# Kernel tuning notes

Measured on AMD Instinct MI355X. Metric: run time of the kernel, lower is better.

## Reference

```python
import jax, jax.numpy as jnp
import numpy as np

N = 100000      # nodes (cells)
E = 1600000     # edges (kNN graph, avg degree 16)
DIM_IN = 128    # input features per cell
H = 8           # heads
C1 = 8          # per-head channels, layer 1 (concat -> 64)
DIM_OUT = 10    # classes (concat=False -> mean over heads)
NEG_SLOPE = 0.2


def setup_inputs() -> dict:
    key = jax.random.key(0)
    ks = jax.random.split(key, 10)
    s = 0.1
    return {
        "x": jax.random.normal(ks[0], (N, DIM_IN), dtype=jnp.float32),
        "edge_index": jax.random.randint(ks[1], (2, E), 0, N, dtype=jnp.int64),
        "W1": jax.random.normal(ks[2], (DIM_IN, H * C1), dtype=jnp.float32) * s,
        "a_src1": jax.random.normal(ks[3], (H, C1), dtype=jnp.float32) * s,
        "a_dst1": jax.random.normal(ks[4], (H, C1), dtype=jnp.float32) * s,
        "b1": jnp.zeros((H * C1,), dtype=jnp.float32),
        "W2": jax.random.normal(ks[5], (H * C1, H * DIM_OUT), dtype=jnp.float32) * s,
        "a_src2": jax.random.normal(ks[6], (H, DIM_OUT), dtype=jnp.float32) * s,
        "a_dst2": jax.random.normal(ks[7], (H, DIM_OUT), dtype=jnp.float32) * s,
        "b2": jnp.zeros((DIM_OUT,), dtype=jnp.float32),
    }


def _gat_layer(x, src, dst, W, a_src, a_dst, bias, concat, n):
    """PyG-style GATConv: gather -> edge attention -> segment softmax -> scatter."""
    h_, c_ = a_src.shape
    h = (x @ W).reshape(n, h_, c_)                       # [N, H, C]
    alpha_s = jnp.einsum('nhc,hc->nh', h, a_src)         # [N, H]
    alpha_d = jnp.einsum('nhc,hc->nh', h, a_dst)         # [N, H]
    # per-edge logits; PyG: message from src j to dst i, softmax over dst
    e = jax.nn.leaky_relu(alpha_s[src] + alpha_d[dst], NEG_SLOPE)  # [E, H]
    e_max = jax.ops.segment_max(e, dst, num_segments=n)            # [N, H]
    e = jnp.exp(e - e_max[dst])
    denom = jax.ops.segment_sum(e, dst, num_segments=n)            # [N, H]
    alpha = e / denom[dst]                                          # [E, H]
    msg = h[src] * alpha[:, :, None]                                # [E, H, C]
    out = jax.ops.segment_sum(msg, dst, num_segments=n)             # [N, H, C]
    out = out.reshape(n, h_ * c_) if concat else out.mean(axis=1)
    return out + bias


def reference(x, edge_index, W1, a_src1, a_dst1, b1, W2, a_src2, a_dst2, b2):
    n = x.shape[0]
    loops = jnp.arange(n, dtype=edge_index.dtype)
    src = jnp.concatenate([edge_index[0], loops])  # PyG adds self-loops by default
    dst = jnp.concatenate([edge_index[1], loops])
    h = _gat_layer(x, src, dst, W1, a_src1, a_dst1, b1, True, n)   # [N, 64]
    h = jax.nn.elu(h)
    h = _gat_layer(h, src, dst, W2, a_src2, a_dst2, b2, False, n)  # [N, dim_out]
    return jax.nn.log_softmax(h, axis=1)
```

## Files before the change

### kernel.cpp

```cpp
#include <hip/hip_runtime.h>
#include <hip/hip_bf16.h>
#include <cstdint>

#define CAP 64
#define SLICES 8
#define CHUNK_EDGES 8192

__device__ __forceinline__ float lrelu(float v) { return fmaxf(v, 0.2f * v); }

typedef float f32x2 __attribute__((ext_vector_type(2)));
__device__ __forceinline__ float2 q2f(unsigned short u) {
    f32x2 v = __builtin_amdgcn_cvt_pk_f32_fp8((int)u, false);
    return make_float2(v.x, v.y);
}
__device__ __forceinline__ int f2q4(float a, float b, float c, float d) {
    int p = __builtin_amdgcn_cvt_pk_fp8_f32(a, b, 0, false);
    p = __builtin_amdgcn_cvt_pk_fp8_f32(c, d, p, true);
    return p;
}
__device__ __forceinline__ float b2f(unsigned short u) { return __uint_as_float(((unsigned)u) << 16); }
__device__ __forceinline__ unsigned short f2b(float f) {
    unsigned u = __float_as_uint(f);
    return (unsigned short)((u + 0x7FFFu + ((u >> 16) & 1u)) >> 16);
}

__global__ __launch_bounds__(256, 8) void k_bg(const int* __restrict__ ei, int E, int N,
                                               int* __restrict__ cnt, int* __restrict__ bucket,
                                               const float* __restrict__ x,
                                               const float* __restrict__ W,
                                               const float* __restrict__ asrc,
                                               const float* __restrict__ adst,
                                               unsigned char* __restrict__ h1q,
                                               float* __restrict__ als, float* __restrict__ ald,
                                               int buildBlocks) {
    __shared__ float xs[32 * 132];
    if ((int)blockIdx.x < buildBlocks) {
        const int s = blockIdx.x & (SLICES - 1);
        const int chunk = blockIdx.x >> 3;
        const int sliceN = (N + SLICES - 1) / SLICES;
        const int lo = s * sliceN;
        const int hi = min(N, lo + sliceN);
        const int base = chunk * CHUNK_EDGES;
        const int end = min(base + CHUNK_EDGES, E);
        for (int e0 = base + (int)threadIdx.x * 4; e0 < end; e0 += 1024) {
            if (e0 + 4 <= end) {
                int4 d = *(const int4*)(ei + E + e0);
                int4 sv = *(const int4*)(ei + e0);
                if (d.x >= lo && d.x < hi) { int a = atomicAdd(&cnt[d.x], 1); if (a < CAP) bucket[(size_t)d.x * CAP + a] = sv.x; }
                if (d.y >= lo && d.y < hi) { int a = atomicAdd(&cnt[d.y], 1); if (a < CAP) bucket[(size_t)d.y * CAP + a] = sv.y; }
                if (d.z >= lo && d.z < hi) { int a = atomicAdd(&cnt[d.z], 1); if (a < CAP) bucket[(size_t)d.z * CAP + a] = sv.z; }
                if (d.w >= lo && d.w < hi) { int a = atomicAdd(&cnt[d.w], 1); if (a < CAP) bucket[(size_t)d.w * CAP + a] = sv.w; }
            } else {
                for (int e = e0; e < end; ++e) {
                    int d = ei[E + e];
                    if (d >= lo && d < hi) {
                        int a = atomicAdd(&cnt[d], 1);
                        if (a < CAP) bucket[(size_t)d * CAP + a] = ei[e];
                    }
                }
            }
        }
        return;
    }
    const int t = threadIdx.x;
    const int rowBase = ((int)blockIdx.x - buildBlocks) * 32;
#pragma unroll
    for (int i = 0; i < 4; ++i) {
        int g = i * 256 + t;
        int r = g >> 5, c4 = (g & 31) << 2;
        float4 v = make_float4(0.f, 0.f, 0.f, 0.f);
        int row = rowBase + r;
        if (row < N) v = *(const float4*)(x + (size_t)row * 128 + c4);
        *(float4*)(&xs[r * 132 + c4]) = v;
    }
    __syncthreads();
    const int tx = t & 15;
    const int ty = t >> 4;
    float acc[2][4] = {};
#pragma unroll 2
    for (int kc = 0; kc < 32; ++kc) {
        float4 a[2];
#pragma unroll
        for (int i = 0; i < 2; ++i) a[i] = *(const float4*)(&xs[(2 * ty + i) * 132 + kc * 4]);
        float4 w[4];
#pragma unroll
        for (int kk = 0; kk < 4; ++kk) w[kk] = *(const float4*)(W + (size_t)(kc * 4 + kk) * 64 + tx * 4);
#pragma unroll
        for (int i = 0; i < 2; ++i) {
            const float* ai = (const float*)&a[i];
#pragma unroll
            for (int j = 0; j < 4; ++j) {
                acc[i][j] += ai[0] * ((const float*)&w[0])[j]
                           + ai[1] * ((const float*)&w[1])[j]
                           + ai[2] * ((const float*)&w[2])[j]
                           + ai[3] * ((const float*)&w[3])[j];
            }
        }
    }
    const int h = tx >> 1;
    float4 av = *(const float4*)(asrc + tx * 4);
    float4 dv = *(const float4*)(adst + tx * 4);
#pragma unroll
    for (int i = 0; i < 2; ++i) {
        int row = rowBase + 2 * ty + i;
        float ps = acc[i][0] * av.x + acc[i][1] * av.y + acc[i][2] * av.z + acc[i][3] * av.w;
        float pd = acc[i][0] * dv.x + acc[i][1] * dv.y + acc[i][2] * dv.z + acc[i][3] * dv.w;
        ps += __shfl_xor(ps, 1);
        pd += __shfl_xor(pd, 1);
        if (row < N) {
            *(int*)(h1q + (size_t)row * 64 + tx * 4) = f2q4(acc[i][0], acc[i][1], acc[i][2], acc[i][3]);
            if ((tx & 1) == 0) {
                als[(size_t)row * 8 + h] = ps;
                ald[(size_t)row * 8 + h] = pd;
            }
        }
    }
}

__global__ __launch_bounds__(256) void k_gemm2(const float* __restrict__ hin,
                                               const float* __restrict__ W,
                                               const float* __restrict__ asrc,
                                               const float* __restrict__ adst,
                                               unsigned char* __restrict__ h2q,
                                               float* __restrict__ ald, int N) {
    __shared__ float xs[64 * 68];
    __shared__ float wt[80 * 68];
    const int t = threadIdx.x;
    const int rowBase = blockIdx.x * 64;
#pragma unroll
    for (int i = 0; i < 4; ++i) {
        int g = i * 256 + t;
        int r = g >> 4, c4 = (g & 15) << 2;
        float4 v = make_float4(0.f, 0.f, 0.f, 0.f);
        int row = rowBase + r;
        if (row < N) v = *(const float4*)(hin + (size_t)row * 64 + c4);
        *(float4*)(&xs[r * 68 + c4]) = v;
    }
#pragma unroll
    for (int i = 0; i < 20; ++i) {
        int g = i * 256 + t;
        int k = g / 80, c = g % 80;
        wt[c * 68 + k] = W[g];
    }
    __syncthreads();
    const int tx = t & 15;
    const int ty = t >> 4;
    float acc[4][5] = {};
#pragma unroll 4
    for (int kc = 0; kc < 16; ++kc) {
        float4 a[4];
#pragma unroll
        for (int i = 0; i < 4; ++i) a[i] = *(const float4*)(&xs[(4 * ty + i) * 68 + kc * 4]);
        float4 w[5];
#pragma unroll
        for (int j = 0; j < 5; ++j) w[j] = *(const float4*)(&wt[(5 * tx + j) * 68 + kc * 4]);
#pragma unroll
        for (int i = 0; i < 4; ++i) {
#pragma unroll
            for (int j = 0; j < 5; ++j) {
                acc[i][j] += a[i].x * w[j].x + a[i].y * w[j].y + a[i].z * w[j].z + a[i].w * w[j].w;
            }
        }
    }
    const int h = tx >> 1;
    float a2[5], d2[5];
#pragma unroll
    for (int j = 0; j < 5; ++j) { a2[j] = asrc[tx * 5 + j]; d2[j] = adst[tx * 5 + j]; }
    __syncthreads();
    unsigned char* qs = (unsigned char*)xs;
#pragma unroll
    for (int i = 0; i < 4; ++i) {
        int row = rowBase + 4 * ty + i;
        float ps = 0.f, pd = 0.f;
#pragma unroll
        for (int j = 0; j < 5; ++j) { ps += acc[i][j] * a2[j]; pd += acc[i][j] * d2[j]; }
        ps += __shfl_xor(ps, 1);
        pd += __shfl_xor(pd, 1);
        int p0 = __builtin_amdgcn_cvt_pk_fp8_f32(acc[i][0], acc[i][1], 0, false);
        int p1 = __builtin_amdgcn_cvt_pk_fp8_f32(acc[i][2], acc[i][3], 0, false);
        int p2 = __builtin_amdgcn_cvt_pk_fp8_f32(acc[i][4], acc[i][4], 0, false);
        unsigned char* q = qs + (4 * ty + i) * 96 + h * 12 + (tx & 1) * 5;
        q[0] = (unsigned char)(p0 & 0xFF);
        q[1] = (unsigned char)((p0 >> 8) & 0xFF);
        q[2] = (unsigned char)(p1 & 0xFF);
        q[3] = (unsigned char)((p1 >> 8) & 0xFF);
        q[4] = (unsigned char)(p2 & 0xFF);
        if ((tx & 1) == 0) {
            *(unsigned short*)(qs + (size_t)(4 * ty + i) * 96 + h * 12 + 10) = f2b(ps);
            if (row < N) ald[(size_t)row * 8 + h] = pd;
        }
    }
    __syncthreads();
    for (int g = t; g < 1536; g += 256) {
        int row = g / 24;
        if (rowBase + row < N)
            *(unsigned int*)(h2q + (size_t)rowBase * 96 + (size_t)g * 4) = ((unsigned int*)qs)[g];
    }
}

__global__ __launch_bounds__(256) void k_agg1(const int* __restrict__ cnt, const int* __restrict__ bucket,
                                              const unsigned char* __restrict__ h1q,
                                              const float* __restrict__ als, const float* __restrict__ ald,
                                              const float* __restrict__ b1,
                                              float* __restrict__ helu, int N) {
    int w = threadIdx.x >> 6, lane = threadIdx.x & 63;
    int e = lane >> 3, h = lane & 7;
    int n = blockIdx.x * 4 + w;
    bool act = n < N;
    float acc[8] = {};
    float den = 0.f;
    if (act) {
        float aldh = ald[(size_t)n * 8 + h];
        auto proc = [&](int s) {
            const unsigned char* row = h1q + (size_t)s * 64 + h * 8;
            int m0 = *(const int*)(row);
            int m1 = *(const int*)(row + 4);
            float a_s = als[(size_t)s * 8 + h];
            float wl = __expf(lrelu(a_s + aldh));
            den += wl;
            f32x2 v;
            v = __builtin_amdgcn_cvt_pk_f32_fp8(m0, false); acc[0] += wl * v.x; acc[1] += wl * v.y;
            v = __builtin_amdgcn_cvt_pk_f32_fp8(m0, true);  acc[2] += wl * v.x; acc[3] += wl * v.y;
            v = __builtin_amdgcn_cvt_pk_f32_fp8(m1, false); acc[4] += wl * v.x; acc[5] += wl * v.y;
            v = __builtin_amdgcn_cvt_pk_f32_fp8(m1, true);  acc[6] += wl * v.x; acc[7] += wl * v.y;
        };
        if (e == 0) proc(n);
        int k = min(cnt[n], CAP);
        const int* bp = bucket + (size_t)n * CAP;
        int i = e;
        int s = (i < k) ? bp[i] : -1;
        while (i < k) {
            int inext = i + 8;
            int snext = (inext < k) ? bp[inext] : -1;
            proc(s);
            i = inext; s = snext;
        }
    }
#pragma unroll
    for (int off = 8; off < 64; off <<= 1) {
        den += __shfl_xor(den, off);
#pragma unroll
        for (int j = 0; j < 8; ++j) acc[j] += __shfl_xor(acc[j], off);
    }
    if (act && e == 0) {
        float inv = 1.f / den;
        float o[8];
#pragma unroll
        for (int j = 0; j < 8; ++j) {
            float v = acc[j] * inv + b1[h * 8 + j];
            o[j] = v > 0.f ? v : __expf(v) - 1.f;
        }
        *(float4*)(helu + (size_t)n * 64 + h * 8)     = make_float4(o[0], o[1], o[2], o[3]);
        *(float4*)(helu + (size_t)n * 64 + h * 8 + 4) = make_float4(o[4], o[5], o[6], o[7]);
    }
}

__global__ __launch_bounds__(256) void k_agg2(const int* __restrict__ cnt, const int* __restrict__ bucket,
                                              const unsigned char* __restrict__ h2q,
                                              const float* __restrict__ ald,
                                              const float* __restrict__ b2,
                                              float* __restrict__ out, int N) {
    __shared__ float sm[4][80];
    int w = threadIdx.x >> 6, lane = threadIdx.x & 63;
    int e = lane >> 3, h = lane & 7;
    int n = blockIdx.x * 4 + w;
    bool act = n < N;
    float acc[10] = {};
    float den = 0.f;
    if (act) {
        float aldh = ald[(size_t)n * 8 + h];
        auto proc = [&](const unsigned char* row) {
            int m0 = *(const int*)(row);
            int m1 = *(const int*)(row + 4);
            int m2 = *(const int*)(row + 8);
            float a_s = b2f((unsigned short)(((unsigned)m2) >> 16));
            float wl = __expf(lrelu(a_s + aldh));
            den += wl;
            f32x2 v;
            v = __builtin_amdgcn_cvt_pk_f32_fp8(m0, false); acc[0] += wl * v.x; acc[1] += wl * v.y;
            v = __builtin_amdgcn_cvt_pk_f32_fp8(m0, true);  acc[2] += wl * v.x; acc[3] += wl * v.y;
            v = __builtin_amdgcn_cvt_pk_f32_fp8(m1, false); acc[4] += wl * v.x; acc[5] += wl * v.y;
            v = __builtin_amdgcn_cvt_pk_f32_fp8(m1, true);  acc[6] += wl * v.x; acc[7] += wl * v.y;
            v = __builtin_amdgcn_cvt_pk_f32_fp8(m2, false); acc[8] += wl * v.x; acc[9] += wl * v.y;
        };
        if (e == 0) proc(h2q + (size_t)n * 96 + h * 12);
        int k = min(cnt[n], CAP);
        const int* bp = bucket + (size_t)n * CAP;
        int i = e;
        int s = (i < k) ? bp[i] : -1;
        while (i < k) {
            int inext = i + 8;
            int snext = (inext < k) ? bp[inext] : -1;
            proc(h2q + (size_t)s * 96 + h * 12);
            i = inext; s = snext;
        }
    }
#pragma unroll
    for (int off = 8; off < 64; off <<= 1) {
        den += __shfl_xor(den, off);
#pragma unroll
        for (int j = 0; j < 10; ++j) acc[j] += __shfl_xor(acc[j], off);
    }
    if (act && e == 0) {
        float inv = 1.f / den;
#pragma unroll
        for (int j = 0; j < 10; ++j) sm[w][h * 10 + j] = acc[j] * inv;
    }
    __syncthreads();
    float m = 0.f;
    if (act && lane < 10) {
#pragma unroll
        for (int hh = 0; hh < 8; ++hh) m += sm[w][hh * 10 + lane];
        m = m * 0.125f + b2[lane];
    }
    __syncthreads();
    if (act && lane < 10) sm[w][lane] = m;
    __syncthreads();
    if (act && lane < 10) {
        float mx = -1e30f;
#pragma unroll
        for (int c = 0; c < 10; ++c) mx = fmaxf(mx, sm[w][c]);
        float ssum = 0.f;
#pragma unroll
        for (int c = 0; c < 10; ++c) ssum += __expf(sm[w][c] - mx);
        out[(size_t)n * 10 + lane] = m - mx - __logf(ssum);
    }
}

extern "C" void kernel_launch(void* const* d_in, const int* in_sizes, int n_in,
                              void* d_out, int out_size, void* d_ws, size_t ws_size,
                              hipStream_t stream) {
    const float* x     = (const float*)d_in[0];
    const int*   ei    = (const int*)d_in[1];
    const float* W1    = (const float*)d_in[2];
    const float* asrc1 = (const float*)d_in[3];
    const float* adst1 = (const float*)d_in[4];
    const float* b1    = (const float*)d_in[5];
    const float* W2    = (const float*)d_in[6];
    const float* asrc2 = (const float*)d_in[7];
    const float* adst2 = (const float*)d_in[8];
    const float* b2    = (const float*)d_in[9];
    float* out = (float*)d_out;

    int N = in_sizes[0] / 128;
    int E = in_sizes[1] / 2;

    char* base = (char*)d_ws;
    size_t off = 0;
    auto alloc = [&](size_t bytes) {
        char* p = base + off;
        off = (off + bytes + 255) & ~(size_t)255;
        return p;
    };
    int*            cnt    = (int*)alloc((size_t)N * 4);
    int*            bucket = (int*)alloc((size_t)N * CAP * 4);
    float*          helu   = (float*)alloc((size_t)N * 64 * 4);
    unsigned char*  hq     = (unsigned char*)alloc((size_t)N * 96);
    float*          als    = (float*)alloc((size_t)N * 8 * 4);
    float*          ald    = (float*)alloc((size_t)N * 8 * 4);
    (void)ws_size; (void)n_in; (void)out_size;

    (void)hipMemsetAsync(cnt, 0, (size_t)N * 4, stream);
    int chunks = (E + CHUNK_EDGES - 1) / CHUNK_EDGES;
    int buildBlocks = chunks * SLICES;
    int gemmBlocks = (N + 31) / 32;
    k_bg<<<buildBlocks + gemmBlocks, 256, 0, stream>>>(ei, E, N, cnt, bucket,
                                                       x, W1, asrc1, adst1, hq, als, ald, buildBlocks);
    k_agg1<<<(N + 3) / 4, 256, 0, stream>>>(cnt, bucket, hq, als, ald, b1, helu, N);
    k_gemm2<<<(N + 63) / 64, 256, 0, stream>>>(helu, W2, asrc2, adst2, hq, ald, N);
    k_agg2<<<(N + 3) / 4, 256, 0, stream>>>(cnt, bucket, hq, ald, b2, out, N);
}
```

Before: 356.9 us.

## Replace slice-filtered bucket build with two-pass partition then scatter

The old build had every slice block re-read all edges and filter by destination range, so the edge list was read eight times. Now a partition kernel reads edges once, bins them by destination slice in shared memory and appends them to per-slice streams. A scatter kernel then does the per-node atomics from those streams, keeping atomics localized per slice. GEMM1 is split out of the fused build kernel into its own launch, which loses the overlap between build and GEMM and adds an intermediate stream buffer pass through memory. The per-slice capacity is sized as E/SLICES plus a fixed margin, which assumes destinations are spread roughly evenly across slices.

Result: slower. 398.3 us (+11.6%).

```diff
diff --git a/kernel.cpp b/kernel.cpp
--- a/kernel.cpp
+++ b/kernel.cpp
@@ -4,15 +4,10 @@
 
 #define CAP 64
 #define SLICES 8
-#define CHUNK_EDGES 8192
 
 __device__ __forceinline__ float lrelu(float v) { return fmaxf(v, 0.2f * v); }
 
 typedef float f32x2 __attribute__((ext_vector_type(2)));
-__device__ __forceinline__ float2 q2f(unsigned short u) {
-    f32x2 v = __builtin_amdgcn_cvt_pk_f32_fp8((int)u, false);
-    return make_float2(v.x, v.y);
-}
 __device__ __forceinline__ int f2q4(float a, float b, float c, float d) {
     int p = __builtin_amdgcn_cvt_pk_fp8_f32(a, b, 0, false);
     p = __builtin_amdgcn_cvt_pk_fp8_f32(c, d, p, true);
@@ -24,46 +19,77 @@
     return (unsigned short)((u + 0x7FFFu + ((u >> 16) & 1u)) >> 16);
 }
 
-__global__ __launch_bounds__(256, 8) void k_bg(const int* __restrict__ ei, int E, int N,
-                                               int* __restrict__ cnt, int* __restrict__ bucket,
-                                               const float* __restrict__ x,
-                                               const float* __restrict__ W,
-                                               const float* __restrict__ asrc,
-                                               const float* __restrict__ adst,
-                                               unsigned char* __restrict__ h1q,
-                                               float* __restrict__ als, float* __restrict__ ald,
-                                               int buildBlocks) {
+__global__ __launch_bounds__(256) void k_part(const int* __restrict__ ei, int E, float inv, int cap,
+                                              int* __restrict__ soff, int2* __restrict__ streams) {
+    __shared__ int2 buf[SLICES][1024];
+    __shared__ int bcnt[SLICES], fcnt[SLICES], gbase[SLICES];
+    const int t = threadIdx.x;
+    for (int base = blockIdx.x * 1024; base < E; base += gridDim.x * 1024) {
+        if (t < SLICES) bcnt[t] = 0;
+        __syncthreads();
+        int e0 = base + t * 4;
+        if (e0 + 4 <= E) {
+            int4 sv = *(const int4*)(ei + e0);
+            int4 dv = *(const int4*)(ei + E + e0);
+            int ss[4] = {sv.x, sv.y, sv.z, sv.w};
+            int ds[4] = {dv.x, dv.y, dv.z, dv.w};
+#pragma unroll
+            for (int j = 0; j < 4; ++j) {
+                int s = min(SLICES - 1, (int)((float)ds[j] * inv));
+                int p = atomicAdd(&bcnt[s], 1);
+                buf[s][p] = make_int2(ss[j], ds[j]);
+            }
+        } else {
+            for (int e = e0; e < E; ++e) {
+                int d = ei[E + e];
+                int s = min(SLICES - 1, (int)((float)d * inv));
+                int p = atomicAdd(&bcnt[s], 1);
+                buf[s][p] = make_int2(ei[e], d);
+            }
+        }
+        __syncthreads();
+        if (t < SLICES) { fcnt[t] = bcnt[t]; gbase[t] = atomicAdd(&soff[t], bcnt[t]); }
+        __syncthreads();
+#pragma unroll
+        for (int s = 0; s < SLICES; ++s) {
+            int c = fcnt[s], g = gbase[s];
+            int2* dst = streams + (size_t)s * cap + g;
+            for (int i = t; i < c; i += 256) dst[i] = buf[s][i];
+        }
+        __syncthreads();
+    }
+}
+
+__global__ __launch_bounds__(256) void k_scatter(const int2* __restrict__ streams,
+                                                 const int* __restrict__ soff, int cap,
+                                                 int* __restrict__ cnt, int* __restrict__ bucket) {
+    int s = blockIdx.x & (SLICES - 1);
+    int blk = blockIdx.x >> 3, nb = gridDim.x >> 3;
+    int tot = soff[s];
+    const int2* st = streams + (size_t)s * cap;
+    for (int base = blk * 1024; base < tot; base += nb * 1024) {
+        int i0 = base + (int)threadIdx.x * 4;
+#pragma unroll
+        for (int j = 0; j < 4; ++j) {
+            int i = i0 + j;
+            if (i < tot) {
+                int2 e = st[i];
+                int a = atomicAdd(&cnt[e.y], 1);
+                if (a < CAP) bucket[(size_t)e.y * CAP + a] = e.x;
+            }
+        }
+    }
+}
+
+__global__ __launch_bounds__(256, 8) void k_gemm1(const float* __restrict__ x,
+                                                  const float* __restrict__ W,
+                                                  const float* __restrict__ asrc,
+                                                  const float* __restrict__ adst,
+                                                  unsigned char* __restrict__ h1q,
+                                                  float* __restrict__ als, float* __restrict__ ald, int N) {
     __shared__ float xs[32 * 132];
-    if ((int)blockIdx.x < buildBlocks) {
-        const int s = blockIdx.x & (SLICES - 1);
-        const int chunk = blockIdx.x >> 3;
-        const int sliceN = (N + SLICES - 1) / SLICES;
-        const int lo = s * sliceN;
-        const int hi = min(N, lo + sliceN);
-        const int base = chunk * CHUNK_EDGES;
-        const int end = min(base + CHUNK_EDGES, E);
-        for (int e0 = base + (int)threadIdx.x * 4; e0 < end; e0 += 1024) {
-            if (e0 + 4 <= end) {
-                int4 d = *(const int4*)(ei + E + e0);
-                int4 sv = *(const int4*)(ei + e0);
-                if (d.x >= lo && d.x < hi) { int a = atomicAdd(&cnt[d.x], 1); if (a < CAP) bucket[(size_t)d.x * CAP + a] = sv.x; }
-                if (d.y >= lo && d.y < hi) { int a = atomicAdd(&cnt[d.y], 1); if (a < CAP) bucket[(size_t)d.y * CAP + a] = sv.y; }
-                if (d.z >= lo && d.z < hi) { int a = atomicAdd(&cnt[d.z], 1); if (a < CAP) bucket[(size_t)d.z * CAP + a] = sv.z; }
-                if (d.w >= lo && d.w < hi) { int a = atomicAdd(&cnt[d.w], 1); if (a < CAP) bucket[(size_t)d.w * CAP + a] = sv.w; }
-            } else {
-                for (int e = e0; e < end; ++e) {
-                    int d = ei[E + e];
-                    if (d >= lo && d < hi) {
-                        int a = atomicAdd(&cnt[d], 1);
-                        if (a < CAP) bucket[(size_t)d * CAP + a] = ei[e];
-                    }
-                }
-            }
-        }
-        return;
-    }
     const int t = threadIdx.x;
-    const int rowBase = ((int)blockIdx.x - buildBlocks) * 32;
+    const int rowBase = blockIdx.x * 32;
 #pragma unroll
     for (int i = 0; i < 4; ++i) {
         int g = i * 256 + t;
@@ -344,6 +370,9 @@
 
     int N = in_sizes[0] / 128;
     int E = in_sizes[1] / 2;
+    int sliceN = (N + SLICES - 1) / SLICES;
+    float inv = 1.0f / (float)sliceN;
+    int cap = E / SLICES + 16384;
 
     char* base = (char*)d_ws;
     size_t off = 0;
@@ -352,20 +381,21 @@
         off = (off + bytes + 255) & ~(size_t)255;
         return p;
     };
-    int*            cnt    = (int*)alloc((size_t)N * 4);
-    int*            bucket = (int*)alloc((size_t)N * CAP * 4);
-    float*          helu   = (float*)alloc((size_t)N * 64 * 4);
-    unsigned char*  hq     = (unsigned char*)alloc((size_t)N * 96);
-    float*          als    = (float*)alloc((size_t)N * 8 * 4);
-    float*          ald    = (float*)alloc((size_t)N * 8 * 4);
+    int*            cnt     = (int*)alloc((size_t)N * 4);
+    int*            soff    = (int*)alloc(SLICES * 4);
+    int*            bucket  = (int*)alloc((size_t)N * CAP * 4);
+    int2*           streams = (int2*)alloc((size_t)SLICES * cap * 8);
+    float*          helu    = (float*)alloc((size_t)N * 64 * 4);
+    unsigned char*  hq      = (unsigned char*)alloc((size_t)N * 96);
+    float*          als     = (float*)alloc((size_t)N * 8 * 4);
+    float*          ald     = (float*)alloc((size_t)N * 8 * 4);
     (void)ws_size; (void)n_in; (void)out_size;
 
     (void)hipMemsetAsync(cnt, 0, (size_t)N * 4, stream);
-    int chunks = (E + CHUNK_EDGES - 1) / CHUNK_EDGES;
-    int buildBlocks = chunks * SLICES;
-    int gemmBlocks = (N + 31) / 32;
-    k_bg<<<buildBlocks + gemmBlocks, 256, 0, stream>>>(ei, E, N, cnt, bucket,
-                                                       x, W1, asrc1, adst1, hq, als, ald, buildBlocks);
+    (void)hipMemsetAsync(soff, 0, SLICES * 4, stream);
+    k_part<<<512, 256, 0, stream>>>(ei, E, inv, cap, soff, streams);
+    k_scatter<<<320, 256, 0, stream>>>(streams, soff, cap, cnt, bucket);
+    k_gemm1<<<(N + 31) / 32, 256, 0, stream>>>(x, W1, asrc1, adst1, hq, als, ald, N);
     k_agg1<<<(N + 3) / 4, 256, 0, stream>>>(cnt, bucket, hq, als, ald, b1, helu, N);
     k_gemm2<<<(N + 63) / 64, 256, 0, stream>>>(helu, W2, asrc2, adst2, hq, ald, N);
     k_agg2<<<(N + 3) / 4, 256, 0, stream>>>(cnt, bucket, hq, ald, b2, out, N);
```
